# Performance work log

Hardware: AMD Instinct MI355X
Metric: run time of the kernel (lower is better)

## Reference

```python
import jax, jax.numpy as jnp
import numpy as np


def setup_inputs() -> dict:
    key = jax.random.key(0)
    x = jax.random.normal(key, (8, 512, 16384), dtype=jnp.float32)
    return {"x": x}


def reference(x) -> jnp.ndarray:
    # Cumulative average along the last (time) axis:
    # y[..., t] = mean(x[..., :t+1]) = cumsum(x)[..., t] / (t+1)
    T = x.shape[-1]
    counts = jnp.arange(1, T + 1, dtype=x.dtype)  # [T]
    return jnp.cumsum(x, axis=-1) / counts
```

## Files before the change

kernel.cpp:

```cpp
#include <hip/hip_runtime.h>


#define ROW_T   16384
#define THREADS 256
#define VEC     4
#define TILE    (THREADS * VEC)
#define NT      (ROW_T / TILE)
#define NWAVES  (THREADS / 64)

typedef float f32x4 __attribute__((ext_vector_type(4)));

__global__ __launch_bounds__(THREADS)
void cumavg_kernel(const float* __restrict__ x, float* __restrict__ y) {
    const int  row  = blockIdx.x;
    const long base = (long)row * ROW_T;
    const int  tid  = threadIdx.x;
    const int  lane = tid & 63;
    const int  wave = tid >> 6;

    __shared__ float wsum[NT][NWAVES];

    const float* px = x + base + (long)tid * VEC;
    float*       py = y + base + (long)tid * VEC;

    f32x4 v[NT];
    #pragma unroll
    for (int t = 0; t < NT; ++t)
        v[t] = *reinterpret_cast<const f32x4*>(px + t * TILE);

    float ts[NT];
    #pragma unroll
    for (int t = 0; t < NT; ++t)
        ts[t] = (v[t].x + v[t].y) + (v[t].z + v[t].w);

    float inc[NT];
    #pragma unroll
    for (int t = 0; t < NT; ++t) inc[t] = ts[t];

    #pragma unroll
    for (int d = 1; d < 64; d <<= 1) {
        #pragma unroll
        for (int t = 0; t < NT; ++t) {
            float n = __shfl_up(inc[t], d, 64);
            if (lane >= d) inc[t] += n;
        }
    }

    if (lane == 63) {
        #pragma unroll
        for (int t = 0; t < NT; ++t) wsum[t][wave] = inc[t];
    }
    __syncthreads();

    float run = 0.0f;
    #pragma unroll
    for (int t = 0; t < NT; ++t) {
        float woff = 0.0f, tot = 0.0f;
        #pragma unroll
        for (int w = 0; w < NWAVES; ++w) {
            float s = wsum[t][w];
            tot  += s;
            woff += (w < wave) ? s : 0.0f;
        }

        float ex = run + woff + (inc[t] - ts[t]);

        const int off = t * TILE + tid * VEC;
        float s0 = ex + v[t].x;
        float s1 = s0 + v[t].y;
        float s2 = s1 + v[t].z;
        float s3 = s2 + v[t].w;

        f32x4 o;
        o.x = s0 * __builtin_amdgcn_rcpf((float)(off + 1));
        o.y = s1 * __builtin_amdgcn_rcpf((float)(off + 2));
        o.z = s2 * __builtin_amdgcn_rcpf((float)(off + 3));
        o.w = s3 * __builtin_amdgcn_rcpf((float)(off + 4));

        __builtin_nontemporal_store(o, reinterpret_cast<f32x4*>(py + t * TILE));

        run += tot;
    }
}

extern "C" void kernel_launch(void* const* d_in, const int* in_sizes, int n_in,
                              void* d_out, int out_size, void* d_ws, size_t ws_size,
                              hipStream_t stream) {
    const float* x = (const float*)d_in[0];
    float*       y = (float*)d_out;
    const int rows = in_sizes[0] / ROW_T;
    hipLaunchKernelGGL(cumavg_kernel, dim3(rows), dim3(THREADS), 0, stream, x, y);
}
```

Measured before the change: 455.4 us.

## Split row scan into chunk-sum and scan-output kernels for finer parallelism

Replaces the one-block-per-row cumulative average with two kernels. The first computes per-chunk sums into workspace, and the second rescans each chunk using the preceding chunk totals as offsets. This aims to increase block count and reduce per-thread register footprint for better latency hiding, at the cost of reading the input twice and an extra launch.

```diff
diff --git a/kernel.cpp b/kernel.cpp
--- a/kernel.cpp
+++ b/kernel.cpp
@@ -2,92 +2,144 @@
 
 
 #define ROW_T   16384
+#define CHUNK   1024
+#define NCH     (ROW_T / CHUNK)
+#define KPB     4
 #define THREADS 256
-#define VEC     4
-#define TILE    (THREADS * VEC)
-#define NT      (ROW_T / TILE)
 #define NWAVES  (THREADS / 64)
 
 typedef float f32x4 __attribute__((ext_vector_type(4)));
 
 __global__ __launch_bounds__(THREADS)
-void cumavg_kernel(const float* __restrict__ x, float* __restrict__ y) {
-    const int  row  = blockIdx.x;
-    const long base = (long)row * ROW_T;
-    const int  tid  = threadIdx.x;
-    const int  lane = tid & 63;
-    const int  wave = tid >> 6;
+void chunksum_kernel(const float* __restrict__ x, float* __restrict__ part) {
+    const int  bid   = blockIdx.x;
+    const long gbase = (long)bid * (KPB * CHUNK);
+    const int  pbase = bid * KPB;
+    const int  tid   = threadIdx.x;
+    const int  lane  = tid & 63;
+    const int  wave  = tid >> 6;
 
-    __shared__ float wsum[NT][NWAVES];
+    __shared__ float wsum[KPB][NWAVES];
 
-    const float* px = x + base + (long)tid * VEC;
-    float*       py = y + base + (long)tid * VEC;
+    f32x4 v[KPB];
+    #pragma unroll
+    for (int k = 0; k < KPB; ++k)
+        v[k] = *reinterpret_cast<const f32x4*>(x + gbase + k * CHUNK + tid * 4);
 
-    f32x4 v[NT];
+    float ts[KPB];
     #pragma unroll
-    for (int t = 0; t < NT; ++t)
-        v[t] = *reinterpret_cast<const f32x4*>(px + t * TILE);
-
-    float ts[NT];
-    #pragma unroll
-    for (int t = 0; t < NT; ++t)
-        ts[t] = (v[t].x + v[t].y) + (v[t].z + v[t].w);
-
-    float inc[NT];
-    #pragma unroll
-    for (int t = 0; t < NT; ++t) inc[t] = ts[t];
+    for (int k = 0; k < KPB; ++k)
+        ts[k] = (v[k].x + v[k].y) + (v[k].z + v[k].w);
 
     #pragma unroll
     for (int d = 1; d < 64; d <<= 1) {
         #pragma unroll
-        for (int t = 0; t < NT; ++t) {
-            float n = __shfl_up(inc[t], d, 64);
-            if (lane >= d) inc[t] += n;
+        for (int k = 0; k < KPB; ++k)
+            ts[k] += __shfl_xor(ts[k], d, 64);
+    }
+
+    if (lane == 0) {
+        #pragma unroll
+        for (int k = 0; k < KPB; ++k) wsum[k][wave] = ts[k];
+    }
+    __syncthreads();
+
+    if (tid < KPB) {
+        float s = 0.0f;
+        #pragma unroll
+        for (int w = 0; w < NWAVES; ++w) s += wsum[tid][w];
+        part[pbase + tid] = s;
+    }
+}
+
+__global__ __launch_bounds__(THREADS)
+void scanout_kernel(const float* __restrict__ x, const float* __restrict__ part,
+                    float* __restrict__ y) {
+    const int  bid   = blockIdx.x;
+    const long gbase = (long)bid * (KPB * CHUNK);
+    const int  c0    = (bid * KPB) & (NCH - 1);
+    const int  prow  = (bid * KPB) & ~(NCH - 1);
+    const int  tid   = threadIdx.x;
+    const int  lane  = tid & 63;
+    const int  wave  = tid >> 6;
+
+    __shared__ float wsum[KPB][NWAVES];
+
+    f32x4 v[KPB];
+    #pragma unroll
+    for (int k = 0; k < KPB; ++k)
+        v[k] = *reinterpret_cast<const f32x4*>(x + gbase + k * CHUNK + tid * 4);
+
+    float pall[NCH];
+    #pragma unroll
+    for (int c = 0; c < NCH; ++c) pall[c] = part[prow + c];
+
+    float offk[KPB];
+    #pragma unroll
+    for (int k = 0; k < KPB; ++k) {
+        float o = 0.0f;
+        #pragma unroll
+        for (int c = 0; c < NCH; ++c) o += (c < c0 + k) ? pall[c] : 0.0f;
+        offk[k] = o;
+    }
+
+    float ts[KPB], inc[KPB];
+    #pragma unroll
+    for (int k = 0; k < KPB; ++k) {
+        ts[k]  = (v[k].x + v[k].y) + (v[k].z + v[k].w);
+        inc[k] = ts[k];
+    }
+    #pragma unroll
+    for (int d = 1; d < 64; d <<= 1) {
+        #pragma unroll
+        for (int k = 0; k < KPB; ++k) {
+            float n = __shfl_up(inc[k], d, 64);
+            if (lane >= d) inc[k] += n;
         }
     }
 
     if (lane == 63) {
         #pragma unroll
-        for (int t = 0; t < NT; ++t) wsum[t][wave] = inc[t];
+        for (int k = 0; k < KPB; ++k) wsum[k][wave] = inc[k];
     }
     __syncthreads();
 
-    float run = 0.0f;
     #pragma unroll
-    for (int t = 0; t < NT; ++t) {
-        float woff = 0.0f, tot = 0.0f;
+    for (int k = 0; k < KPB; ++k) {
+        float woff = 0.0f;
         #pragma unroll
-        for (int w = 0; w < NWAVES; ++w) {
-            float s = wsum[t][w];
-            tot  += s;
-            woff += (w < wave) ? s : 0.0f;
-        }
+        for (int w = 0; w < NWAVES; ++w)
+            woff += (w < wave) ? wsum[k][w] : 0.0f;
 
-        float ex = run + woff + (inc[t] - ts[t]);
+        float ex = offk[k] + woff + (inc[k] - ts[k]);
 
-        const int off = t * TILE + tid * VEC;
-        float s0 = ex + v[t].x;
-        float s1 = s0 + v[t].y;
-        float s2 = s1 + v[t].z;
-        float s3 = s2 + v[t].w;
+        const float pf = (float)((c0 + k) * CHUNK + tid * 4);
+
+        float s0 = ex + v[k].x;
+        float s1 = s0 + v[k].y;
+        float s2 = s1 + v[k].z;
+        float s3 = s2 + v[k].w;
 
         f32x4 o;
-        o.x = s0 * __builtin_amdgcn_rcpf((float)(off + 1));
-        o.y = s1 * __builtin_amdgcn_rcpf((float)(off + 2));
-        o.z = s2 * __builtin_amdgcn_rcpf((float)(off + 3));
-        o.w = s3 * __builtin_amdgcn_rcpf((float)(off + 4));
+        o.x = s0 * __builtin_amdgcn_rcpf(pf + 1.0f);
+        o.y = s1 * __builtin_amdgcn_rcpf(pf + 2.0f);
+        o.z = s2 * __builtin_amdgcn_rcpf(pf + 3.0f);
+        o.w = s3 * __builtin_amdgcn_rcpf(pf + 4.0f);
 
-        __builtin_nontemporal_store(o, reinterpret_cast<f32x4*>(py + t * TILE));
-
-        run += tot;
+        __builtin_nontemporal_store(o, reinterpret_cast<f32x4*>(y + gbase + k * CHUNK + tid * 4));
     }
 }
 
 extern "C" void kernel_launch(void* const* d_in, const int* in_sizes, int n_in,
                               void* d_out, int out_size, void* d_ws, size_t ws_size,
                               hipStream_t stream) {
-    const float* x = (const float*)d_in[0];
-    float*       y = (float*)d_out;
-    const int rows = in_sizes[0] / ROW_T;
-    hipLaunchKernelGGL(cumavg_kernel, dim3(rows), dim3(THREADS), 0, stream, x, y);
+    const float* x    = (const float*)d_in[0];
+    float*       y    = (float*)d_out;
+    float*       part = (float*)d_ws;
+
+    const long total = in_sizes[0];
+    const int  nblk  = (int)(total / (KPB * CHUNK));
+
+    hipLaunchKernelGGL(chunksum_kernel, dim3(nblk), dim3(THREADS), 0, stream, x, part);
+    hipLaunchKernelGGL(scanout_kernel,  dim3(nblk), dim3(THREADS), 0, stream, x, part, y);
 }
```

Result: no change. 464.5 us (+2.0%).
